# Optimization experiments

Hardware: AMD Instinct MI355X
Metric: run time of the kernel (lower is better)

Reference implementation:

```python
import jax, jax.numpy as jnp
import numpy as np

E, TOP, C, H, W, B = 8, 2, 128, 96, 96, 8
NUM_GATES = 4
KH = 3  # capsule conv kernel


def setup_inputs() -> dict:
    key = jax.random.key(0)
    ks = jax.random.split(key, 6)
    x = jax.random.normal(ks[0], (B, C, H, W), jnp.float32)
    # xavier_uniform for gates: bound = sqrt(6/(fan_in+fan_out))
    bound = float(np.sqrt(6.0 / (C + E)))
    G = jax.random.uniform(ks[1], (NUM_GATES, C, E), jnp.float32, -bound, bound)
    # per-expert capsule convs: the 16 parallel (C->capsule_dim) 3x3 convs are
    # stacked along the output-channel axis into one (C->C) conv per expert
    Wc = jax.random.normal(ks[2], (E, C, C, KH, KH), jnp.float32) * (1.0 / np.sqrt(C * KH * KH))
    bc = jax.random.normal(ks[3], (E, C), jnp.float32) * 0.01
    # 1x1 output projection per expert
    Wp = jax.random.normal(ks[4], (E, C, C), jnp.float32) * (1.0 / np.sqrt(C))
    bp = jax.random.normal(ks[5], (E, C), jnp.float32) * 0.01
    return {"x": x, "G": G, "Wc": Wc, "bc": bc, "Wp": Wp, "bp": bp}


def _squash(u):
    # squash over the full channel dim (dim=1), matching the torch module
    sn = jnp.sum(u * u, axis=1, keepdims=True)
    return (sn / (1.0 + sn)) * u / jnp.sqrt(sn + 1e-8)


def _expert(x, wc, bc, wp, bp):
    u = jax.lax.conv_general_dilated(
        x, wc, window_strides=(1, 1), padding='SAME',
        dimension_numbers=('NCHW', 'OIHW', 'NCHW')) + bc[None, :, None, None]
    u = jax.nn.relu(u)
    u = _squash(u)
    return jnp.einsum('bchw,oc->bohw', u, wp) + bp[None, :, None, None]


def _cv_squared(v):
    v = v.astype(jnp.float32)
    return jnp.var(v, ddof=1) / (jnp.mean(v) ** 2 + 1e-10)


def reference(x, G, Wc, bc, Wp, bp):
    Bn = x.shape[0]
    # run every expert on the full batch (dense equivalent of the masked dispatch)
    y_all = jax.vmap(lambda wc_, bc_, wp_, bp_: _expert(x, wc_, bc_, wp_, bp_))(
        Wc, bc, Wp, bp)  # [E, B, C, H, W]
    x_gap = jnp.mean(x, axis=(2, 3))  # [B, C]  (adaptive avg pool to 1x1)
    ys, losses = [], []
    for g in range(NUM_GATES):
        probs = jax.nn.softmax(x_gap @ G[g], axis=1)           # [B, E]
        tv, ti = jax.lax.top_k(probs, TOP)                     # [B, TOP]
        tw = jax.nn.softmax(tv, axis=1)                        # renormalized top-k weights
        out = jnp.zeros_like(x)
        for k in range(TOP):
            y_sel = y_all[ti[:, k], jnp.arange(Bn)]            # gather per-sample expert out
            out = out + y_sel * tw[:, k][:, None, None, None]
        ys.append(out)
        losses.append(_cv_squared(jnp.sum(probs, axis=0)))     # cv^2 of expert usage
    total_loss = jnp.mean(jnp.stack(losses))
    return (*ys, total_loss)
```

## Files before the change

kernel.cpp:

```cpp
#include <hip/hip_runtime.h>
#include <math.h>

#define CHW 9216
#define OPG 9437184

typedef unsigned short u16;
typedef __attribute__((ext_vector_type(8))) short short8;
typedef __attribute__((ext_vector_type(4))) float f32x4;

#define WS_XT  8192
#define WS_AT  18882560
#define WS_WPT 21241856

__device__ __forceinline__ u16 f2bf(float f) {
    unsigned u = __float_as_uint(f);
    u += 0x7fff + ((u >> 16) & 1);
    return (u16)(u >> 16);
}

__device__ __forceinline__ void gload_lds16(const void* g, void* l) {
    __builtin_amdgcn_global_load_lds(
        (const __attribute__((address_space(1))) void*)g,
        (__attribute__((address_space(3))) void*)l, 16, 0, 0);
}

__global__ void gap_kernel(const float* __restrict__ x, float* __restrict__ xgap) {
    int bc = blockIdx.x;
    const float* p = x + (size_t)bc * CHW;
    float s = 0.f;
    for (int i = threadIdx.x; i < CHW; i += 256) s += p[i];
    __shared__ float red[256];
    red[threadIdx.x] = s;
    __syncthreads();
    for (int off = 128; off > 0; off >>= 1) {
        if (threadIdx.x < off) red[threadIdx.x] += red[threadIdx.x + off];
        __syncthreads();
    }
    if (threadIdx.x == 0) xgap[bc] = red[0] * (1.0f / 9216.0f);
}

__global__ void gate_kernel(const float* __restrict__ G, float* __restrict__ ws,
                            float* __restrict__ loss_out) {
    __shared__ float gap_s[1024];
    __shared__ float logits[64];
    __shared__ float probs[64];
    __shared__ float vsum[8];
    __shared__ float losses[4];
    int t = threadIdx.x;
    for (int i = t; i < 1024; i += 64) gap_s[i] = ws[i];
    int b = t >> 3, e = t & 7;
    int* iw = (int*)(ws + 1344);
    float* wt = ws + 1408;
    __syncthreads();
    for (int g = 0; g < 4; ++g) {
        float acc = 0.f;
        const float* Gg = G + g * 1024;
        for (int c = 0; c < 128; ++c) acc += gap_s[b * 128 + c] * Gg[c * 8 + e];
        logits[t] = acc;
        __syncthreads();
        float m = -1e30f;
        for (int j = 0; j < 8; ++j) m = fmaxf(m, logits[b * 8 + j]);
        float den = 0.f;
        for (int j = 0; j < 8; ++j) den += expf(logits[b * 8 + j] - m);
        float pr = expf(acc - m) / den;
        probs[t] = pr;
        __syncthreads();
        if (e == 0) {
            int i0 = 0; float v0 = probs[b * 8];
            for (int j = 1; j < 8; ++j) { float v = probs[b * 8 + j]; if (v > v0) { v0 = v; i0 = j; } }
            int i1 = -1; float v1 = -1e30f;
            for (int j = 0; j < 8; ++j) { if (j == i0) continue; float v = probs[b * 8 + j]; if (v > v1) { v1 = v; i1 = j; } }
            float r = expf(v1 - v0);
            float inv = 1.f / (1.f + r);
            iw[g * 16 + b * 2 + 0] = i0;
            iw[g * 16 + b * 2 + 1] = i1;
            wt[g * 16 + b * 2 + 0] = inv;
            wt[g * 16 + b * 2 + 1] = r * inv;
        }
        if (t < 8) {
            float v = 0.f;
            for (int bb = 0; bb < 8; ++bb) v += probs[bb * 8 + t];
            vsum[t] = v;
        }
        __syncthreads();
        if (t == 0) {
            float mean = 0.f;
            for (int j = 0; j < 8; ++j) mean += vsum[j];
            mean *= 0.125f;
            float var = 0.f;
            for (int j = 0; j < 8; ++j) { float d = vsum[j] - mean; var += d * d; }
            var *= (1.f / 7.f);
            losses[g] = var / (mean * mean + 1e-10f);
        }
        __syncthreads();
    }
    if (t == 0) loss_out[0] = 0.25f * (losses[0] + losses[1] + losses[2] + losses[3]);
}

__global__ void pre_x(const float* __restrict__ x, u16* __restrict__ Xt) {
    int h = blockIdx.x, b = blockIdx.y, t = threadIdx.x;
    __shared__ u16 lds[12288];
    const float* xb = x + ((size_t)b * 128) * CHW + h * 96;
    for (int i = t; i < 12288; i += 256) {
        int c = i / 96, w = i - c * 96;
        lds[(c >> 6) * 6144 + w * 64 + ((c & 63) ^ ((w & 7) << 3))] = f2bf(xb[(size_t)c * CHW + w]);
    }
    __syncthreads();
    const unsigned* l32 = (const unsigned*)lds;
    unsigned* o32 = (unsigned*)Xt;
    for (int i = t; i < 6144; i += 256) {
        int hf = (i >= 3072) ? 1 : 0;
        int rem = i - hf * 3072;
        o32[((size_t)(b * 2 + hf) * 96 + h) * 3072 + rem] = l32[i];
    }
}

__global__ void pre_wc2(const float* __restrict__ Wc, u16* __restrict__ At2) {
    int idx = blockIdx.x * 256 + threadIdx.x;
    int s = idx & 7;
    int lane = (idx >> 3) & 63;
    int mb = (idx >> 9) & 3;
    int mi = (idx >> 11) & 1;
    int ck = (idx >> 12) & 1;
    int rem = idx >> 13;
    int r = rem % 9;
    int rem2 = rem / 9;
    int hf = rem2 & 1;
    int e = rem2 >> 1;
    int l15 = lane & 15, quad = lane >> 4;
    int o = mi * 64 + mb * 16 + l15;
    int cin = hf * 64 + ck * 32 + quad * 8 + s;
    size_t src = (((size_t)e * 128 + o) * 128 + cin) * 9 + r;
    At2[idx] = f2bf(Wc[src]);
}

__global__ void pre_wp(const float* __restrict__ Wp, u16* __restrict__ Wpt) {
    int i = blockIdx.x * 256 + threadIdx.x;
    if (i < 131072) Wpt[i] = f2bf(Wp[i]);
}

__launch_bounds__(512, 2)
__global__ void expert_kernel(const u16* __restrict__ Xt, const u16* __restrict__ At2,
                              const u16* __restrict__ Wpt,
                              const float* __restrict__ bc, const float* __restrict__ bp,
                              const float* __restrict__ ws, float* __restrict__ out) {
    int hs = blockIdx.x, b = blockIdx.y, g = blockIdx.z;
    int h0 = hs * 2;
    int t = threadIdx.x, lane = t & 63, wv = t >> 6;
    int mi = wv & 1, ni = wv >> 1;
    int l15 = lane & 15, quad = lane >> 4, q8 = quad * 8;
    int nrow = ni >> 1;
    int ncb = (ni & 1) * 48;

    const int* iw = (const int*)(ws + 1344);
    const float* wt = ws + 1408;
    int ee[2];
    float wwt[2];
    ee[0] = iw[g * 16 + b * 2 + 0]; ee[1] = iw[g * 16 + b * 2 + 1];
    wwt[0] = wt[g * 16 + b * 2 + 0]; wwt[1] = wt[g * 16 + b * 2 + 1];

    __shared__ __align__(16) char smem[99328];
    u16* Hs = (u16*)smem;
    float* part_s = (float*)smem;
    u16* v_s = (u16*)(smem + 9216);

    f32x4 zero = {0.f, 0.f, 0.f, 0.f};
    f32x4 acc[2][12];
    #pragma unroll
    for (int i = 0; i < 12; ++i) { acc[0][i] = zero; acc[1][i] = zero; }

    int abase = mi * 2048 + lane * 8;

    const u16* Ab0 = At2 + (size_t)(ee[0] * 2) * 73728;
    const u16* Ab1 = At2 + (size_t)(ee[1] * 2) * 73728;

    #define ASRC(P, U) ((P) + ((U) >= 18 ? 73728 + ((U) - 18) * 4096 : (U) * 4096))
    #define STAGE(U) { u16* ab_ = (u16*)(smem + 50176 + ((U) % 3) * 16384);          \
                       gload_lds16(ASRC(Ab0, (U)) + t * 8, ab_ + t * 8);             \
                       gload_lds16(ASRC(Ab1, (U)) + t * 8, ab_ + 4096 + t * 8); }
    #define RD_AF(DST, G, XOFF) { const u16* abr_ = (const u16*)(smem + 50176 + ((G) % 3) * 16384) + (XOFF); \
        _Pragma("unroll") for (int mb_ = 0; mb_ < 4; ++mb_) DST[mb_] = *(const short8*)(abr_ + abase + mb_ * 512); }
    #define RD_BV(DST, G) { const int s_ = (G) % 18, r_ = s_ >> 1, ck_ = s_ & 1;     \
        const int dyi_ = r_ / 3, dxi_ = r_ - dyi_ * 3, hb_ = (nrow + dyi_) * 12544;  \
        _Pragma("unroll") for (int j_ = 0; j_ < 3; ++j_) {                           \
            int col_ = ncb + j_ * 16 + l15 + dxi_;                                   \
            int ba_ = hb_ + col_ * 128 + ((q8 ^ (((col_ - 1) & 7) << 3)) << 1);      \
            DST[j_] = *(const short8*)(smem + (ba_ ^ (ck_ << 6))); } }
    #define MFMA12(XP, AF, BV) { _Pragma("unroll") for (int mb_ = 0; mb_ < 4; ++mb_) \
        _Pragma("unroll") for (int j_ = 0; j_ < 3; ++j_)                             \
            acc[XP][mb_ * 3 + j_] = __builtin_amdgcn_mfma_f32_16x16x32_bf16(AF[mb_], BV[j_], acc[XP][mb_ * 3 + j_], 0, 0, 0); }
    #define SBAR() __builtin_amdgcn_sched_barrier(0)

    {
        uint4 z; z.x = z.y = z.z = z.w = 0u;
        #pragma unroll
        for (int rr = 0; rr < 4; ++rr) {
            int row = h0 - 1 + rr;
            if (row < 0 || row >= 96)
                for (int i = t; i < 784; i += 512) *(uint4*)(Hs + rr * 6272 + i * 8) = z;
        }
        if (t < 64) {
            int rr = t >> 4, cs = (t >> 3) & 1, p = t & 7;
            *(uint4*)(Hs + rr * 6272 + cs * 97 * 64 + p * 8) = z;
        }
        const u16* Xb = Xt + (size_t)(b * 2 + 0) * 96 * 6144;
        #pragma unroll
        for (int rr = 0; rr < 4; ++rr) {
            int row = h0 - 1 + rr;
            if (row >= 0 && row < 96) {
                const u16* src = Xb + (size_t)row * 6144;
                u16* dst = Hs + rr * 6272 + 64;
                for (int i = t; i < 768; i += 512) gload_lds16(src + i * 8, dst + i * 8);
            }
        }
    }
    STAGE(0); STAGE(1);
    __syncthreads();

    short8 af0[4], af1[4], bvA[3], bvB[3];

    #pragma unroll
    for (int hf = 0; hf < 2; ++hf) {
        if (hf == 1) {
            const u16* Xb = Xt + (size_t)(b * 2 + 1) * 96 * 6144;
            #pragma unroll
            for (int rr = 0; rr < 4; ++rr) {
                int row = h0 - 1 + rr;
                if (row >= 0 && row < 96) {
                    const u16* src = Xb + (size_t)row * 6144;
                    u16* dst = Hs + rr * 6272 + 64;
                    for (int i = t; i < 768; i += 512) gload_lds16(src + i * 8, dst + i * 8);
                }
            }
            asm volatile("s_waitcnt vmcnt(0)" ::: "memory");
            __builtin_amdgcn_s_barrier();
        }
        RD_AF(af0, hf * 18, 0);
        RD_BV(bvA, hf * 18);

        #pragma unroll
        for (int u = 0; u < 18; ++u) {
            const int gg = hf * 18 + u;
            if (gg + 2 <= 35) STAGE(gg + 2);
            RD_AF(af1, gg, 4096);
            SBAR();
            __builtin_amdgcn_s_setprio(1);
            if (u & 1) { MFMA12(0, af0, bvB); } else { MFMA12(0, af0, bvA); }
            __builtin_amdgcn_s_setprio(0);
            SBAR();
            if (u < 17) {
                if (u & 1) { RD_BV(bvA, gg + 1); } else { RD_BV(bvB, gg + 1); }
                RD_AF(af0, gg + 1, 0);
            }
            SBAR();
            __builtin_amdgcn_s_setprio(1);
            if (u & 1) { MFMA12(1, af1, bvB); } else { MFMA12(1, af1, bvA); }
            __builtin_amdgcn_s_setprio(0);
            asm volatile("s_waitcnt vmcnt(0)" ::: "memory");
            if (u == 17) asm volatile("s_waitcnt lgkmcnt(0)" ::: "memory");
            __builtin_amdgcn_s_barrier();
        }
    }
    #undef STAGE
    #undef ASRC
    #undef RD_AF
    #undef RD_BV
    #undef MFMA12
    #undef SBAR

    #pragma unroll
    for (int xp = 0; xp < 2; ++xp) {
        int e_ = ee[xp];
        __syncthreads();
        #pragma unroll
        for (int j = 0; j < 3; ++j) {
            int n = ni * 48 + j * 16 + l15;
            float ssum = 0.f;
            #pragma unroll
            for (int mb = 0; mb < 4; ++mb) {
                f32x4 a = acc[xp][mb * 3 + j];
                #pragma unroll
                for (int rg = 0; rg < 4; ++rg) {
                    float u = fmaxf(a[rg] + bc[e_ * 128 + mi * 64 + mb * 16 + quad * 4 + rg], 0.f);
                    a[rg] = u; ssum += u * u;
                }
                acc[xp][mb * 3 + j] = a;
            }
            part_s[n * 12 + mi * 4 + quad] = ssum;
        }
        __syncthreads();
        #pragma unroll
        for (int j = 0; j < 3; ++j) {
            int n = ni * 48 + j * 16 + l15;
            f32x4 p0 = *(const f32x4*)(part_s + n * 12);
            f32x4 p1 = *(const f32x4*)(part_s + n * 12 + 4);
            float sn2 = p0[0] + p0[1] + p0[2] + p0[3] + p1[0] + p1[1] + p1[2] + p1[3];
            float fsj = sn2 / ((1.f + sn2) * sqrtf(sn2 + 1e-8f));
            int sw = (n & 7) << 3;
            #pragma unroll
            for (int mb = 0; mb < 4; ++mb) {
                f32x4 a = acc[xp][mb * 3 + j];
                short4 pk;
                pk.x = (short)f2bf(a[0] * fsj); pk.y = (short)f2bf(a[1] * fsj);
                pk.z = (short)f2bf(a[2] * fsj); pk.w = (short)f2bf(a[3] * fsj);
                int cb = mb * 16 + quad * 4;
                *(short4*)(v_s + n * 128 + ((cb ^ sw) | (mi << 6))) = pk;
            }
        }
        __syncthreads();
        #pragma unroll
        for (int i = 0; i < 12; ++i) acc[xp][i] = zero;
        const u16* We_ = Wpt + (size_t)e_ * 16384;
        #pragma unroll
        for (int kk = 0; kk < 4; ++kk) {
            short8 af[4];
            #pragma unroll
            for (int mb = 0; mb < 4; ++mb)
                af[mb] = *(const short8*)(We_ + (mi * 64 + mb * 16 + l15) * 128 + kk * 32 + q8);
            short8 bvv[3];
            #pragma unroll
            for (int j = 0; j < 3; ++j) {
                int n = ni * 48 + j * 16 + l15;
                int sw = (n & 7) << 3;
                int pos = ((kk & 2) << 5) | ((((kk & 1) << 5) + q8) ^ sw);
                bvv[j] = *(const short8*)(v_s + n * 128 + pos);
            }
            #pragma unroll
            for (int mb = 0; mb < 4; ++mb)
                #pragma unroll
                for (int j = 0; j < 3; ++j)
                    acc[xp][mb * 3 + j] = __builtin_amdgcn_mfma_f32_16x16x32_bf16(af[mb], bvv[j], acc[xp][mb * 3 + j], 0, 0, 0);
        }
    }

    int row = h0 + nrow;
    #pragma unroll
    for (int mb = 0; mb < 4; ++mb)
        #pragma unroll
        for (int rg = 0; rg < 4; ++rg) {
            int o = mi * 64 + mb * 16 + quad * 4 + rg;
            float y0b = bp[ee[0] * 128 + o];
            float y1b = bp[ee[1] * 128 + o];
            size_t obase = (size_t)g * OPG + ((size_t)(b * 128 + o)) * CHW + (size_t)row * 96;
            #pragma unroll
            for (int j = 0; j < 3; ++j) {
                float y0 = acc[0][mb * 3 + j][rg] + y0b;
                float y1 = acc[1][mb * 3 + j][rg] + y1b;
                out[obase + ncb + j * 16 + l15] = wwt[0] * y0 + wwt[1] * y1;
            }
        }
}

extern "C" void kernel_launch(void* const* d_in, const int* in_sizes, int n_in,
                              void* d_out, int out_size, void* d_ws, size_t ws_size,
                              hipStream_t stream) {
    const float* x  = (const float*)d_in[0];
    const float* G  = (const float*)d_in[1];
    const float* Wc = (const float*)d_in[2];
    const float* bc = (const float*)d_in[3];
    const float* Wp = (const float*)d_in[4];
    const float* bp = (const float*)d_in[5];
    float* out = (float*)d_out;
    float* ws  = (float*)d_ws;
    u16* Xt  = (u16*)((char*)d_ws + WS_XT);
    u16* At2 = (u16*)((char*)d_ws + WS_AT);
    u16* Wpt = (u16*)((char*)d_ws + WS_WPT);

    gap_kernel<<<dim3(1024), dim3(256), 0, stream>>>(x, ws);
    gate_kernel<<<dim3(1), dim3(64), 0, stream>>>(G, ws, out + (size_t)4 * OPG);
    pre_x<<<dim3(96, 8), dim3(256), 0, stream>>>(x, Xt);
    pre_wc2<<<dim3(4608), dim3(256), 0, stream>>>(Wc, At2);
    pre_wp<<<dim3(512), dim3(256), 0, stream>>>(Wp, Wpt);
    expert_kernel<<<dim3(48, 8, 4), dim3(512), 0, stream>>>(Xt, At2, Wpt, bc, bp, ws, out);
}
```

Before: 423.3 us.

## Fuse prep kernels into one launch and load second expert weights directly to registers

The four preprocessing kernels (GAP, x transpose, Wc repack, Wp convert) are merged into one launch that dispatches on block index, which removes launch gaps. In the expert kernel, only expert 0's conv weights are staged through LDS. Expert 1's A fragments are loaded straight from global memory into registers each step, which cuts the LDS footprint from about 97KB to 73KB. The smaller footprint is meant to let more blocks fit per CU or ease LDS pressure, at the cost of exposed global-load latency on the second MFMA group, which now waits on direct global loads.

Result: slower. 436.3 us (+3.1%).

```diff
diff --git a/kernel.cpp b/kernel.cpp
--- a/kernel.cpp
+++ b/kernel.cpp
@@ -24,19 +24,62 @@
         (__attribute__((address_space(3))) void*)l, 16, 0, 0);
 }
 
-__global__ void gap_kernel(const float* __restrict__ x, float* __restrict__ xgap) {
-    int bc = blockIdx.x;
-    const float* p = x + (size_t)bc * CHW;
-    float s = 0.f;
-    for (int i = threadIdx.x; i < CHW; i += 256) s += p[i];
-    __shared__ float red[256];
-    red[threadIdx.x] = s;
-    __syncthreads();
-    for (int off = 128; off > 0; off >>= 1) {
-        if (threadIdx.x < off) red[threadIdx.x] += red[threadIdx.x + off];
-        __syncthreads();
-    }
-    if (threadIdx.x == 0) xgap[bc] = red[0] * (1.0f / 9216.0f);
+__global__ void prep_kernel(const float* __restrict__ x, u16* __restrict__ Xt,
+                            const float* __restrict__ Wc, u16* __restrict__ At2,
+                            const float* __restrict__ Wp, u16* __restrict__ Wpt,
+                            float* __restrict__ xgap) {
+    __shared__ __align__(16) char pbuf[24576];
+    int bid = blockIdx.x, t = threadIdx.x;
+    if (bid < 1024) {
+        float* red = (float*)pbuf;
+        const float* p = x + (size_t)bid * CHW;
+        float s = 0.f;
+        for (int i = t; i < CHW; i += 256) s += p[i];
+        red[t] = s;
+        __syncthreads();
+        for (int off = 128; off > 0; off >>= 1) {
+            if (t < off) red[t] += red[t + off];
+            __syncthreads();
+        }
+        if (t == 0) xgap[bid] = red[0] * (1.0f / 9216.0f);
+    } else if (bid < 1792) {
+        int idx = bid - 1024;
+        int h = idx % 96, b = idx / 96;
+        u16* lds = (u16*)pbuf;
+        const float* xb = x + ((size_t)b * 128) * CHW + h * 96;
+        for (int i = t; i < 12288; i += 256) {
+            int c = i / 96, w = i - c * 96;
+            lds[(c >> 6) * 6144 + w * 64 + ((c & 63) ^ ((w & 7) << 3))] = f2bf(xb[(size_t)c * CHW + w]);
+        }
+        __syncthreads();
+        const unsigned* l32 = (const unsigned*)lds;
+        unsigned* o32 = (unsigned*)Xt;
+        for (int i = t; i < 6144; i += 256) {
+            int hf = (i >= 3072) ? 1 : 0;
+            int rem = i - hf * 3072;
+            o32[((size_t)(b * 2 + hf) * 96 + h) * 3072 + rem] = l32[i];
+        }
+    } else if (bid < 6400) {
+        int idx = (bid - 1792) * 256 + t;
+        int s = idx & 7;
+        int lane = (idx >> 3) & 63;
+        int mb = (idx >> 9) & 3;
+        int mi = (idx >> 11) & 1;
+        int ck = (idx >> 12) & 1;
+        int rem = idx >> 13;
+        int r = rem % 9;
+        int rem2 = rem / 9;
+        int hf = rem2 & 1;
+        int e = rem2 >> 1;
+        int l15 = lane & 15, quad = lane >> 4;
+        int o = mi * 64 + mb * 16 + l15;
+        int cin = hf * 64 + ck * 32 + quad * 8 + s;
+        size_t src = (((size_t)e * 128 + o) * 128 + cin) * 9 + r;
+        At2[idx] = f2bf(Wc[src]);
+    } else {
+        int i = (bid - 6400) * 256 + t;
+        if (i < 131072) Wpt[i] = f2bf(Wp[i]);
+    }
 }
 
 __global__ void gate_kernel(const float* __restrict__ G, float* __restrict__ ws,
@@ -97,48 +140,6 @@
     if (t == 0) loss_out[0] = 0.25f * (losses[0] + losses[1] + losses[2] + losses[3]);
 }
 
-__global__ void pre_x(const float* __restrict__ x, u16* __restrict__ Xt) {
-    int h = blockIdx.x, b = blockIdx.y, t = threadIdx.x;
-    __shared__ u16 lds[12288];
-    const float* xb = x + ((size_t)b * 128) * CHW + h * 96;
-    for (int i = t; i < 12288; i += 256) {
-        int c = i / 96, w = i - c * 96;
-        lds[(c >> 6) * 6144 + w * 64 + ((c & 63) ^ ((w & 7) << 3))] = f2bf(xb[(size_t)c * CHW + w]);
-    }
-    __syncthreads();
-    const unsigned* l32 = (const unsigned*)lds;
-    unsigned* o32 = (unsigned*)Xt;
-    for (int i = t; i < 6144; i += 256) {
-        int hf = (i >= 3072) ? 1 : 0;
-        int rem = i - hf * 3072;
-        o32[((size_t)(b * 2 + hf) * 96 + h) * 3072 + rem] = l32[i];
-    }
-}
-
-__global__ void pre_wc2(const float* __restrict__ Wc, u16* __restrict__ At2) {
-    int idx = blockIdx.x * 256 + threadIdx.x;
-    int s = idx & 7;
-    int lane = (idx >> 3) & 63;
-    int mb = (idx >> 9) & 3;
-    int mi = (idx >> 11) & 1;
-    int ck = (idx >> 12) & 1;
-    int rem = idx >> 13;
-    int r = rem % 9;
-    int rem2 = rem / 9;
-    int hf = rem2 & 1;
-    int e = rem2 >> 1;
-    int l15 = lane & 15, quad = lane >> 4;
-    int o = mi * 64 + mb * 16 + l15;
-    int cin = hf * 64 + ck * 32 + quad * 8 + s;
-    size_t src = (((size_t)e * 128 + o) * 128 + cin) * 9 + r;
-    At2[idx] = f2bf(Wc[src]);
-}
-
-__global__ void pre_wp(const float* __restrict__ Wp, u16* __restrict__ Wpt) {
-    int i = blockIdx.x * 256 + threadIdx.x;
-    if (i < 131072) Wpt[i] = f2bf(Wp[i]);
-}
-
 __launch_bounds__(512, 2)
 __global__ void expert_kernel(const u16* __restrict__ Xt, const u16* __restrict__ At2,
                               const u16* __restrict__ Wpt,
@@ -159,7 +160,7 @@
     ee[0] = iw[g * 16 + b * 2 + 0]; ee[1] = iw[g * 16 + b * 2 + 1];
     wwt[0] = wt[g * 16 + b * 2 + 0]; wwt[1] = wt[g * 16 + b * 2 + 1];
 
-    __shared__ __align__(16) char smem[99328];
+    __shared__ __align__(16) char smem[74752];
     u16* Hs = (u16*)smem;
     float* part_s = (float*)smem;
     u16* v_s = (u16*)(smem + 9216);
@@ -175,11 +176,12 @@
     const u16* Ab1 = At2 + (size_t)(ee[1] * 2) * 73728;
 
     #define ASRC(P, U) ((P) + ((U) >= 18 ? 73728 + ((U) - 18) * 4096 : (U) * 4096))
-    #define STAGE(U) { u16* ab_ = (u16*)(smem + 50176 + ((U) % 3) * 16384);          \
-                       gload_lds16(ASRC(Ab0, (U)) + t * 8, ab_ + t * 8);             \
-                       gload_lds16(ASRC(Ab1, (U)) + t * 8, ab_ + 4096 + t * 8); }
-    #define RD_AF(DST, G, XOFF) { const u16* abr_ = (const u16*)(smem + 50176 + ((G) % 3) * 16384) + (XOFF); \
+    #define STAGE(U) { u16* ab_ = (u16*)(smem + 50176 + ((U) % 3) * 8192);           \
+                       gload_lds16(ASRC(Ab0, (U)) + t * 8, ab_ + t * 8); }
+    #define RD_AF(DST, G) { const u16* abr_ = (const u16*)(smem + 50176 + ((G) % 3) * 8192); \
         _Pragma("unroll") for (int mb_ = 0; mb_ < 4; ++mb_) DST[mb_] = *(const short8*)(abr_ + abase + mb_ * 512); }
+    #define LD_GA(DST, U) { const u16* ga_ = ASRC(Ab1, (U));                         \
+        _Pragma("unroll") for (int mb_ = 0; mb_ < 4; ++mb_) DST[mb_] = *(const short8*)(ga_ + abase + mb_ * 512); }
     #define RD_BV(DST, G) { const int s_ = (G) % 18, r_ = s_ >> 1, ck_ = s_ & 1;     \
         const int dyi_ = r_ / 3, dxi_ = r_ - dyi_ * 3, hb_ = (nrow + dyi_) * 12544;  \
         _Pragma("unroll") for (int j_ = 0; j_ < 3; ++j_) {                           \
@@ -217,7 +219,7 @@
     STAGE(0); STAGE(1);
     __syncthreads();
 
-    short8 af0[4], af1[4], bvA[3], bvB[3];
+    short8 af0[4], ga1[4], bvA[3], bvB[3];
 
     #pragma unroll
     for (int hf = 0; hf < 2; ++hf) {
@@ -235,14 +237,14 @@
             asm volatile("s_waitcnt vmcnt(0)" ::: "memory");
             __builtin_amdgcn_s_barrier();
         }
-        RD_AF(af0, hf * 18, 0);
+        RD_AF(af0, hf * 18);
         RD_BV(bvA, hf * 18);
 
         #pragma unroll
         for (int u = 0; u < 18; ++u) {
             const int gg = hf * 18 + u;
+            LD_GA(ga1, gg);
             if (gg + 2 <= 35) STAGE(gg + 2);
-            RD_AF(af1, gg, 4096);
             SBAR();
             __builtin_amdgcn_s_setprio(1);
             if (u & 1) { MFMA12(0, af0, bvB); } else { MFMA12(0, af0, bvA); }
@@ -250,11 +252,11 @@
             SBAR();
             if (u < 17) {
                 if (u & 1) { RD_BV(bvA, gg + 1); } else { RD_BV(bvB, gg + 1); }
-                RD_AF(af0, gg + 1, 0);
+                RD_AF(af0, gg + 1);
             }
             SBAR();
             __builtin_amdgcn_s_setprio(1);
-            if (u & 1) { MFMA12(1, af1, bvB); } else { MFMA12(1, af1, bvA); }
+            if (u & 1) { MFMA12(1, ga1, bvB); } else { MFMA12(1, ga1, bvA); }
             __builtin_amdgcn_s_setprio(0);
             asm volatile("s_waitcnt vmcnt(0)" ::: "memory");
             if (u == 17) asm volatile("s_waitcnt lgkmcnt(0)" ::: "memory");
@@ -264,6 +266,7 @@
     #undef STAGE
     #undef ASRC
     #undef RD_AF
+    #undef LD_GA
     #undef RD_BV
     #undef MFMA12
     #undef SBAR
@@ -366,10 +369,7 @@
     u16* At2 = (u16*)((char*)d_ws + WS_AT);
     u16* Wpt = (u16*)((char*)d_ws + WS_WPT);
 
-    gap_kernel<<<dim3(1024), dim3(256), 0, stream>>>(x, ws);
+    prep_kernel<<<dim3(6912), dim3(256), 0, stream>>>(x, Xt, Wc, At2, Wp, Wpt, ws);
     gate_kernel<<<dim3(1), dim3(64), 0, stream>>>(G, ws, out + (size_t)4 * OPG);
-    pre_x<<<dim3(96, 8), dim3(256), 0, stream>>>(x, Xt);
-    pre_wc2<<<dim3(4608), dim3(256), 0, stream>>>(Wc, At2);
-    pre_wp<<<dim3(512), dim3(256), 0, stream>>>(Wp, Wpt);
     expert_kernel<<<dim3(48, 8, 4), dim3(512), 0, stream>>>(Xt, At2, Wpt, bc, bp, ws, out);
 }
```
